# Performance work log

Hardware: AMD Instinct MI355X
Metric: run time of the kernel (lower is better)

The kernel has to match this reference:

```python
import jax, jax.numpy as jnp
import numpy as np

B, IN, OUT = 65536, 1024, 1024
NB, D, H, L = 16, 32, 64, 4      # n_bundles, bundle_dim, norm_mlp hidden, n_latent_layers
TOT = NB * D                      # total latent dim = 512 (also encoder/decoder hidden)


def setup_inputs() -> dict:
    key = jax.random.key(0)
    ks = jax.random.split(key, 20)
    rn = lambda k, shape, s=0.02: (jax.random.normal(k, shape, dtype=jnp.float32) * s)
    return {
        "x": jax.random.normal(ks[0], (B, IN), dtype=jnp.float32),
        # encoder: Linear(IN,TOT), Linear(TOT,TOT), Linear(TOT,TOT)
        "enc_w1": rn(ks[1], (TOT, IN)), "enc_b1": jnp.zeros((TOT,), jnp.float32),
        "enc_w2": rn(ks[2], (TOT, TOT)), "enc_b2": jnp.zeros((TOT,), jnp.float32),
        "enc_w3": rn(ks[3], (TOT, TOT)), "enc_b3": jnp.zeros((TOT,), jnp.float32),
        # per-latent-layer norm_mlp: Linear(NB,H)+b, Linear(H,H)+b, Linear(H,NB) no bias
        "mlp1_w": rn(ks[4], (L, H, NB)), "mlp1_b": jnp.zeros((L, H), jnp.float32),
        "mlp2_w": rn(ks[5], (L, H, H)),  "mlp2_b": jnp.zeros((L, H), jnp.float32),
        "mlp3_w": rn(ks[6], (L, NB, H)),
        # mixing_weights[i][j] has shape (d_i, d_j); homogeneous -> [L,NB,NB,D,D], init 0.01*randn
        "mix_w": rn(ks[7], (L, NB, NB, D, D), 0.01),
        "gate_bias": jnp.zeros((L, NB), jnp.float32),
        # decoder: Linear(TOT,TOT), Linear(TOT,TOT), Linear(TOT,OUT)
        "dec_w1": rn(ks[8], (TOT, TOT)), "dec_b1": jnp.zeros((TOT,), jnp.float32),
        "dec_w2": rn(ks[9], (TOT, TOT)), "dec_b2": jnp.zeros((TOT,), jnp.float32),
        "dec_w3": rn(ks[10], (OUT, TOT)), "dec_b3": jnp.zeros((OUT,), jnp.float32),
    }


def _gelu(v):
    return jax.nn.gelu(v, approximate=False)  # torch nn.GELU default (erf)


def _soft_equivariant(z, m1w, m1b, m2w, m2b, m3w, mw, gb):
    # z: [B, TOT] -> bundles [B, NB, D] (homogeneous dims, contiguous split == reshape)
    zb = z.reshape(z.shape[0], NB, D)
    norms = jnp.linalg.norm(zb, axis=-1) + 1e-8          # [B, NB]
    h = _gelu(norms @ m1w.T + m1b)                        # [B, H]
    h = _gelu(h @ m2w.T + m2b)                            # [B, H]
    scales = jax.nn.softplus(h @ m3w.T)                   # [B, NB]
    equi = zb * scales[:, :, None]                        # [B, NB, D]
    # mixed_i = sum_j F.linear(bundles[j], W[i][j]) = bundles[j] @ W[i][j].T
    mixed = jnp.einsum('bjd,ijed->bie', zb, mw)           # [B, NB, D]
    gates = jax.nn.sigmoid(gb)                            # [NB]
    combined = equi + gates[None, :, None] * mixed        # [B, NB, D]
    return z + combined.reshape(z.shape[0], TOT)          # residual


def reference(x, enc_w1, enc_b1, enc_w2, enc_b2, enc_w3, enc_b3,
              mlp1_w, mlp1_b, mlp2_w, mlp2_b, mlp3_w, mix_w, gate_bias,
              dec_w1, dec_b1, dec_w2, dec_b2, dec_w3, dec_b3):
    # encoder
    z = _gelu(x @ enc_w1.T + enc_b1)
    z = _gelu(z @ enc_w2.T + enc_b2)
    z = z @ enc_w3.T + enc_b3
    # latent dynamics: L SoftEquivariantLayers (fixed small loop over layers)
    for l in range(L):
        z = _soft_equivariant(z, mlp1_w[l], mlp1_b[l], mlp2_w[l], mlp2_b[l],
                              mlp3_w[l], mix_w[l], gate_bias[l])
    # decoder
    y = _gelu(z @ dec_w1.T + dec_b1)
    y = _gelu(y @ dec_w2.T + dec_b2)
    return y @ dec_w3.T + dec_b3
```

## Files before the change

kernel.cpp:

```cpp
#include <hip/hip_runtime.h>
#include <hip/hip_bf16.h>

typedef float f32x4 __attribute__((ext_vector_type(4)));
typedef __bf16 bf16x8 __attribute__((ext_vector_type(8)));
typedef unsigned short u16x8 __attribute__((ext_vector_type(8)));
typedef unsigned short u16;

__device__ __forceinline__ u16 f2bf(float f) {
  __bf16 h = (__bf16)f;
  return __builtin_bit_cast(u16, h);
}
__device__ __forceinline__ float bf2f(u16 s) {
  return __uint_as_float(((unsigned int)s) << 16);
}
__device__ __forceinline__ float gelu_f(float x) {
  return 0.5f * x * (1.0f + erff(x * 0.70710678118654752f));
}
__device__ __forceinline__ void gload_lds16(const void* g, void* l) {
  __builtin_amdgcn_global_load_lds((const __attribute__((address_space(1))) void*)g,
                                   (__attribute__((address_space(3))) void*)l, 16, 0, 0);
}
#define MFMA(a, b, c) __builtin_amdgcn_mfma_f32_16x16x32_bf16((a), (b), (c), 0, 0, 0)
#define BARRIER_PINNED() do { \
    __builtin_amdgcn_s_barrier(); \
    asm volatile("" ::: "memory"); \
    __builtin_amdgcn_sched_barrier(0); \
  } while (0)

__global__ void cvt_all(const float* __restrict__ e1, const float* __restrict__ e2,
                        const float* __restrict__ e3, const float* __restrict__ d1,
                        const float* __restrict__ d2, const float* __restrict__ d3,
                        const float* __restrict__ mx, u16* __restrict__ dst)
{
  int i = blockIdx.x * blockDim.x + threadIdx.x;
  int stride = gridDim.x * blockDim.x;
  for (; i < 3145728; i += stride) {
    float v;
    if (i < 524288)        v = e1[i];
    else if (i < 786432)   v = e2[i - 524288];
    else if (i < 1048576)  v = e3[i - 786432];
    else if (i < 1310720)  v = d1[i - 1048576];
    else if (i < 1572864)  v = d2[i - 1310720];
    else if (i < 2097152)  v = d3[i - 1572864];
    else {
      int j = i - 2097152;
      int l = j >> 18, rem = j & 262143;
      int o = rem >> 9, k = rem & 511;
      int bi = o >> 5, e = o & 31, jj = k >> 5, dd = k & 31;
      v = mx[(((l * 16 + bi) * 16 + jj) * 32 + e) * 32 + dd];
    }
    dst[i] = f2bf(v);
  }
}

__global__ void cvt_x(const float* __restrict__ s, u16* __restrict__ d) {
  int i = blockIdx.x * blockDim.x + threadIdx.x;
  int stride = gridDim.x * blockDim.x;
  for (; i < 8388608; i += stride) {
    float4 v0 = *(const float4*)(s + (size_t)i * 8);
    float4 v1 = *(const float4*)(s + (size_t)i * 8 + 4);
    u16x8 u;
    u[0] = f2bf(v0.x); u[1] = f2bf(v0.y); u[2] = f2bf(v0.z); u[3] = f2bf(v0.w);
    u[4] = f2bf(v1.x); u[5] = f2bf(v1.y); u[6] = f2bf(v1.z); u[7] = f2bf(v1.w);
    *(u16x8*)(d + (size_t)i * 8) = u;
  }
}

template<int EPI>
__global__ __launch_bounds__(512, 2)
void gemm_big(const u16* __restrict__ A, const u16* __restrict__ Bw,
              const float* __restrict__ bias, void* __restrict__ Cp,
              const u16* __restrict__ zOld, const float* __restrict__ scales,
              const float* __restrict__ gateBias, int M, int N, int K)
{
  extern __shared__ char smem[];
  const int tid = threadIdx.x;
  const int lane = tid & 63;
  const int wid = tid >> 6;

  const int nx = N >> 7;
  const int ny = M >> 8;
  const int d = blockIdx.x;
  const int xcd = d & 7;
  const int seq = d >> 3;
  const int by = xcd * (ny >> 3) + seq / nx;
  const int bx = seq - (seq / nx) * nx;
  const int m0 = by << 8;
  const int n0 = bx << 7;

  const int wr = wid >> 2;
  const int wc = wid & 3;
  const int r16 = lane & 15;
  const int kg = (lane >> 4) << 3;
  const int sw = (r16 & 7) << 4;

  const u16* pA[4];
  const u16* pB[2];
  #pragma unroll
  for (int it = 0; it < 4; ++it) {
    int c = ((it * 8 + wid) << 6) + lane;
    int row = c >> 3;
    int cb = (c & 7) << 4;
    pA[it] = A + (size_t)(m0 + row) * K + ((cb ^ ((row & 7) << 4)) >> 1);
  }
  #pragma unroll
  for (int it = 0; it < 2; ++it) {
    int c = ((it * 8 + wid) << 6) + lane;
    int row = c >> 3;
    int cb = (c & 7) << 4;
    pB[it] = Bw + (size_t)(n0 + row) * K + ((cb ^ ((row & 7) << 4)) >> 1);
  }

  auto stage = [&](int kt, int b) {
    char* dstA = smem + b * 49152;
    char* dstB = dstA + 32768;
    const int ko = kt << 6;
    #pragma unroll
    for (int it = 0; it < 4; ++it)
      gload_lds16(pA[it] + ko, dstA + ((it * 8 + wid) << 10));
    #pragma unroll
    for (int it = 0; it < 2; ++it)
      gload_lds16(pB[it] + ko, dstB + ((it * 8 + wid) << 10));
  };

  const int NT = K >> 6;
  f32x4 acc[8][2] = {};

  stage(0, 0);
  stage(1, 1);

  int cb = 0, ib = 2;
  for (int kt = 0; kt < NT; ++kt) {
    if (kt + 1 < NT) { asm volatile("s_waitcnt vmcnt(6)" ::: "memory"); }
    else             { asm volatile("s_waitcnt vmcnt(0)" ::: "memory"); }
    BARRIER_PINNED();

    if (kt + 2 < NT) {
      stage(kt + 2, ib);
      ib = (ib == 2) ? 0 : ib + 1;
    }

    const char* Ac = smem + cb * 49152;
    const char* Bc = Ac + 32768;
    #pragma unroll
    for (int kk = 0; kk < 64; kk += 32) {
      const int kb = ((kk + kg) << 1) ^ sw;
      bf16x8 bv0 = *(const bf16x8*)(Bc + ((wc * 32 + r16) << 7) + kb);
      bf16x8 bv1 = *(const bf16x8*)(Bc + ((wc * 32 + 16 + r16) << 7) + kb);
      #pragma unroll
      for (int mh = 0; mh < 2; ++mh) {
        bf16x8 av[4];
        #pragma unroll
        for (int m = 0; m < 4; ++m)
          av[m] = *(const bf16x8*)(Ac + ((wr * 128 + mh * 64 + m * 16 + r16) << 7) + kb);
        __builtin_amdgcn_s_setprio(1);
        #pragma unroll
        for (int m = 0; m < 4; ++m) {
          acc[mh * 4 + m][0] = MFMA(av[m], bv0, acc[mh * 4 + m][0]);
          acc[mh * 4 + m][1] = MFMA(av[m], bv1, acc[mh * 4 + m][1]);
        }
        __builtin_amdgcn_s_setprio(0);
      }
    }
    cb = (cb == 2) ? 0 : cb + 1;
  }

  const int colBase = n0 + wc * 32 + r16;
  const int rowBase = m0 + wr * 128 + ((lane >> 4) << 2);
  #pragma unroll
  for (int n = 0; n < 2; ++n) {
    const int col = colBase + n * 16;
    float bv_ = 0.f, gate = 0.f;
    if constexpr (EPI == 0 || EPI == 1 || EPI == 3) bv_ = bias[col];
    if constexpr (EPI == 2) gate = 1.f / (1.f + expf(-gateBias[col >> 5]));
    #pragma unroll
    for (int m = 0; m < 8; ++m) {
      #pragma unroll
      for (int r = 0; r < 4; ++r) {
        const int row = rowBase + m * 16 + r;
        float v = acc[m][n][r];
        if constexpr (EPI == 0) {
          ((u16*)Cp)[(size_t)row * N + col] = f2bf(gelu_f(v + bv_));
        } else if constexpr (EPI == 1) {
          ((u16*)Cp)[(size_t)row * N + col] = f2bf(v + bv_);
        } else if constexpr (EPI == 2) {
          float sc = scales[(size_t)row * 16 + (col >> 5)];
          float zo = bf2f(zOld[(size_t)row * 512 + col]);
          ((u16*)Cp)[(size_t)row * N + col] = f2bf(zo * (1.f + sc) + gate * v);
        } else {
          ((float*)Cp)[(size_t)row * N + col] = v + bv_;
        }
      }
    }
  }
}

__global__ __launch_bounds__(256, 2)
void norm_mlp2(const u16* __restrict__ z,
               const float* __restrict__ w1, const float* __restrict__ b1,
               const float* __restrict__ w2, const float* __restrict__ b2,
               const float* __restrict__ w3, float* __restrict__ scales)
{
  __shared__ float nrm[256][17];
  const int tid = threadIdx.x;
  const size_t base = (size_t)blockIdx.x << 8;

  #pragma unroll
  for (int p = 0; p < 16; ++p) {
    const int C = (p << 8) + tid;
    const int r = C >> 4, b = C & 15;
    const u16* zp = z + ((base + r) << 9) + (b << 5);
    float ss = 0.f;
    #pragma unroll
    for (int q = 0; q < 4; ++q) {
      u16x8 v = *(const u16x8*)(zp + q * 8);
      #pragma unroll
      for (int j = 0; j < 8; ++j) { float f = bf2f(v[j]); ss += f * f; }
    }
    nrm[r][b] = sqrtf(ss) + 1e-8f;
  }
  __syncthreads();

  float nr[16];
  #pragma unroll
  for (int i = 0; i < 16; ++i) nr[i] = nrm[tid][i];

  float h2[64];
  #pragma unroll
  for (int j = 0; j < 64; ++j) h2[j] = b2[j];

  for (int kt = 0; kt < 4; ++kt) {
    float h1t[16];
    #pragma unroll
    for (int k16 = 0; k16 < 16; ++k16) {
      const int k = (kt << 4) + k16;
      float t = b1[k];
      #pragma unroll
      for (int i = 0; i < 16; ++i) t += nr[i] * w1[k * 16 + i];
      h1t[k16] = gelu_f(t);
    }
    const float* w2t = w2 + (kt << 4);
    #pragma unroll
    for (int j = 0; j < 64; ++j) {
      float s = 0.f;
      #pragma unroll
      for (int k16 = 0; k16 < 16; ++k16) s += h1t[k16] * w2t[j * 64 + k16];
      h2[j] += s;
    }
  }
  #pragma unroll
  for (int j = 0; j < 64; ++j) h2[j] = gelu_f(h2[j]);

  float* srow = scales + ((base + tid) << 4);
  #pragma unroll
  for (int b = 0; b < 16; ++b) {
    float s = 0.f;
    #pragma unroll
    for (int k = 0; k < 64; ++k) s += h2[k] * w3[b * 64 + k];
    s = (s > 20.f) ? s : log1pf(expf(s));
    srow[b] = s;
  }
}

#define BIG_SMEM 147456

extern "C" void kernel_launch(void* const* d_in, const int* in_sizes, int n_in,
                              void* d_out, int out_size, void* d_ws, size_t ws_size,
                              hipStream_t stream)
{
  (void)in_sizes; (void)n_in; (void)out_size; (void)ws_size;
  const float* x      = (const float*)d_in[0];
  const float* enc_w1 = (const float*)d_in[1];
  const float* enc_b1 = (const float*)d_in[2];
  const float* enc_w2 = (const float*)d_in[3];
  const float* enc_b2 = (const float*)d_in[4];
  const float* enc_w3 = (const float*)d_in[5];
  const float* enc_b3 = (const float*)d_in[6];
  const float* mlp1_w = (const float*)d_in[7];
  const float* mlp1_b = (const float*)d_in[8];
  const float* mlp2_w = (const float*)d_in[9];
  const float* mlp2_b = (const float*)d_in[10];
  const float* mlp3_w = (const float*)d_in[11];
  const float* mix_w  = (const float*)d_in[12];
  const float* gate_b = (const float*)d_in[13];
  const float* dec_w1 = (const float*)d_in[14];
  const float* dec_b1 = (const float*)d_in[15];
  const float* dec_w2 = (const float*)d_in[16];
  const float* dec_b2 = (const float*)d_in[17];
  const float* dec_w3 = (const float*)d_in[18];
  const float* dec_b3 = (const float*)d_in[19];

  char* ws = (char*)d_ws;
  const int M = 65536;

  u16*   xb     = (u16*)ws;
  u16*   zA     = (u16*)(ws + 134217728ULL);
  u16*   zB     = (u16*)ws;
  float* scales = (float*)(ws + 201326592ULL);
  u16*   wBase  = (u16*)(ws + 205520896ULL);
  u16* wE1 = wBase;
  u16* wE2 = wE1 + 524288;
  u16* wE3 = wE2 + 262144;
  u16* wD1 = wE3 + 262144;
  u16* wD2 = wD1 + 262144;
  u16* wD3 = wD2 + 262144;
  u16* wMix = wD3 + 524288;

  hipError_t e;
  e = hipFuncSetAttribute(reinterpret_cast<const void*>(&gemm_big<0>),
                          hipFuncAttributeMaxDynamicSharedMemorySize, BIG_SMEM);
  e = hipFuncSetAttribute(reinterpret_cast<const void*>(&gemm_big<1>),
                          hipFuncAttributeMaxDynamicSharedMemorySize, BIG_SMEM);
  e = hipFuncSetAttribute(reinterpret_cast<const void*>(&gemm_big<2>),
                          hipFuncAttributeMaxDynamicSharedMemorySize, BIG_SMEM);
  e = hipFuncSetAttribute(reinterpret_cast<const void*>(&gemm_big<3>),
                          hipFuncAttributeMaxDynamicSharedMemorySize, BIG_SMEM);
  (void)e;

  cvt_all<<<512, 256, 0, stream>>>(enc_w1, enc_w2, enc_w3, dec_w1, dec_w2, dec_w3,
                                   mix_w, wBase);

  dim3 blk(512);
  const int g512  = 256 * 4;
  const int g1024 = 256 * 8;

  cvt_x<<<2048, 256, 0, stream>>>(x, xb);
  gemm_big<0><<<g512, blk, BIG_SMEM, stream>>>(xb, wE1, enc_b1, zA, nullptr, nullptr, nullptr, M, 512, 1024);
  gemm_big<0><<<g512, blk, BIG_SMEM, stream>>>(zA, wE2, enc_b2, zB, nullptr, nullptr, nullptr, M, 512, 512);
  gemm_big<1><<<g512, blk, BIG_SMEM, stream>>>(zB, wE3, enc_b3, zA, nullptr, nullptr, nullptr, M, 512, 512);

  u16* cur = zA;
  u16* nxt = zB;
  for (int l = 0; l < 4; ++l) {
    norm_mlp2<<<256, dim3(256), 0, stream>>>(cur, mlp1_w + l * 1024, mlp1_b + l * 64,
                                             mlp2_w + l * 4096, mlp2_b + l * 64,
                                             mlp3_w + l * 1024, scales);
    gemm_big<2><<<g512, blk, BIG_SMEM, stream>>>(cur, wMix + (size_t)l * 262144, nullptr, nxt,
                                                 cur, scales, gate_b + l * 16, M, 512, 512);
    u16* t = cur; cur = nxt; nxt = t;
  }

  gemm_big<0><<<g512, blk, BIG_SMEM, stream>>>(cur, wD1, dec_b1, nxt, nullptr, nullptr, nullptr, M, 512, 512);
  { u16* t = cur; cur = nxt; nxt = t; }
  gemm_big<0><<<g512, blk, BIG_SMEM, stream>>>(cur, wD2, dec_b2, nxt, nullptr, nullptr, nullptr, M, 512, 512);
  { u16* t = cur; cur = nxt; nxt = t; }
  gemm_big<3><<<g1024, blk, BIG_SMEM, stream>>>(cur, wD3, dec_b3, d_out, nullptr, nullptr, nullptr, M, 1024, 512);
}
```

Baseline: 1.199 ms.

## Widen GEMM tiles to 256x256 with double buffering and one block per CU

Switches the GEMM from 256x128 tiles with a three-stage LDS pipeline to 256x256 tiles with two-stage double buffering. Each wave now computes a 128x64 output slab with 32 accumulators, which raises MFMA work per LDS load and halves how often the A matrix is re-read from global memory. The cost is one block per CU (launch bounds 512,1), twice the accumulator registers, a full vmcnt(0) wait on every k-step, and fewer blocks in flight, so load latency may be less well hidden.

```diff
diff --git a/kernel.cpp b/kernel.cpp
--- a/kernel.cpp
+++ b/kernel.cpp
@@ -67,18 +67,18 @@
 }
 
 template<int EPI>
-__global__ __launch_bounds__(512, 2)
-void gemm_big(const u16* __restrict__ A, const u16* __restrict__ Bw,
-              const float* __restrict__ bias, void* __restrict__ Cp,
-              const u16* __restrict__ zOld, const float* __restrict__ scales,
-              const float* __restrict__ gateBias, int M, int N, int K)
+__global__ __launch_bounds__(512, 1)
+void gemm_huge(const u16* __restrict__ A, const u16* __restrict__ Bw,
+               const float* __restrict__ bias, void* __restrict__ Cp,
+               const u16* __restrict__ zOld, const float* __restrict__ scales,
+               const float* __restrict__ gateBias, int M, int N, int K)
 {
   extern __shared__ char smem[];
   const int tid = threadIdx.x;
   const int lane = tid & 63;
   const int wid = tid >> 6;
 
-  const int nx = N >> 7;
+  const int nx = N >> 8;
   const int ny = M >> 8;
   const int d = blockIdx.x;
   const int xcd = d & 7;
@@ -86,7 +86,7 @@
   const int by = xcd * (ny >> 3) + seq / nx;
   const int bx = seq - (seq / nx) * nx;
   const int m0 = by << 8;
-  const int n0 = bx << 7;
+  const int n0 = bx << 8;
 
   const int wr = wid >> 2;
   const int wc = wid & 3;
@@ -95,58 +95,49 @@
   const int sw = (r16 & 7) << 4;
 
   const u16* pA[4];
-  const u16* pB[2];
+  const u16* pB[4];
   #pragma unroll
   for (int it = 0; it < 4; ++it) {
     int c = ((it * 8 + wid) << 6) + lane;
     int row = c >> 3;
     int cb = (c & 7) << 4;
     pA[it] = A + (size_t)(m0 + row) * K + ((cb ^ ((row & 7) << 4)) >> 1);
-  }
-  #pragma unroll
-  for (int it = 0; it < 2; ++it) {
-    int c = ((it * 8 + wid) << 6) + lane;
-    int row = c >> 3;
-    int cb = (c & 7) << 4;
     pB[it] = Bw + (size_t)(n0 + row) * K + ((cb ^ ((row & 7) << 4)) >> 1);
   }
 
   auto stage = [&](int kt, int b) {
-    char* dstA = smem + b * 49152;
+    char* dstA = smem + (b << 16);
     char* dstB = dstA + 32768;
     const int ko = kt << 6;
     #pragma unroll
     for (int it = 0; it < 4; ++it)
       gload_lds16(pA[it] + ko, dstA + ((it * 8 + wid) << 10));
     #pragma unroll
-    for (int it = 0; it < 2; ++it)
+    for (int it = 0; it < 4; ++it)
       gload_lds16(pB[it] + ko, dstB + ((it * 8 + wid) << 10));
   };
 
   const int NT = K >> 6;
-  f32x4 acc[8][2] = {};
+  f32x4 acc[8][4] = {};
 
   stage(0, 0);
-  stage(1, 1);
-
-  int cb = 0, ib = 2;
+
   for (int kt = 0; kt < NT; ++kt) {
-    if (kt + 1 < NT) { asm volatile("s_waitcnt vmcnt(6)" ::: "memory"); }
-    else             { asm volatile("s_waitcnt vmcnt(0)" ::: "memory"); }
+    const int cur = kt & 1;
+    asm volatile("s_waitcnt vmcnt(0)" ::: "memory");
     BARRIER_PINNED();
 
-    if (kt + 2 < NT) {
-      stage(kt + 2, ib);
-      ib = (ib == 2) ? 0 : ib + 1;
-    }
-
-    const char* Ac = smem + cb * 49152;
+    if (kt + 1 < NT) stage(kt + 1, cur ^ 1);
+
+    const char* Ac = smem + (cur << 16);
     const char* Bc = Ac + 32768;
     #pragma unroll
     for (int kk = 0; kk < 64; kk += 32) {
       const int kb = ((kk + kg) << 1) ^ sw;
-      bf16x8 bv0 = *(const bf16x8*)(Bc + ((wc * 32 + r16) << 7) + kb);
-      bf16x8 bv1 = *(const bf16x8*)(Bc + ((wc * 32 + 16 + r16) << 7) + kb);
+      bf16x8 bv[4];
+      #pragma unroll
+      for (int n = 0; n < 4; ++n)
+        bv[n] = *(const bf16x8*)(Bc + ((wc * 64 + n * 16 + r16) << 7) + kb);
       #pragma unroll
       for (int mh = 0; mh < 2; ++mh) {
         bf16x8 av[4];
@@ -155,20 +146,19 @@
           av[m] = *(const bf16x8*)(Ac + ((wr * 128 + mh * 64 + m * 16 + r16) << 7) + kb);
         __builtin_amdgcn_s_setprio(1);
         #pragma unroll
-        for (int m = 0; m < 4; ++m) {
-          acc[mh * 4 + m][0] = MFMA(av[m], bv0, acc[mh * 4 + m][0]);
-          acc[mh * 4 + m][1] = MFMA(av[m], bv1, acc[mh * 4 + m][1]);
-        }
+        for (int m = 0; m < 4; ++m)
+          #pragma unroll
+          for (int n = 0; n < 4; ++n)
+            acc[mh * 4 + m][n] = MFMA(av[m], bv[n], acc[mh * 4 + m][n]);
         __builtin_amdgcn_s_setprio(0);
       }
     }
-    cb = (cb == 2) ? 0 : cb + 1;
-  }
-
-  const int colBase = n0 + wc * 32 + r16;
+  }
+
+  const int colBase = n0 + wc * 64 + r16;
   const int rowBase = m0 + wr * 128 + ((lane >> 4) << 2);
   #pragma unroll
-  for (int n = 0; n < 2; ++n) {
+  for (int n = 0; n < 4; ++n) {
     const int col = colBase + n * 16;
     float bv_ = 0.f, gate = 0.f;
     if constexpr (EPI == 0 || EPI == 1 || EPI == 3) bv_ = bias[col];
@@ -262,7 +252,7 @@
   }
 }
 
-#define BIG_SMEM 147456
+#define HUGE_SMEM 131072
 
 extern "C" void kernel_launch(void* const* d_in, const int* in_sizes, int n_in,
                               void* d_out, int out_size, void* d_ws, size_t ws_size,
@@ -307,27 +297,27 @@
   u16* wMix = wD3 + 524288;
 
   hipError_t e;
-  e = hipFuncSetAttribute(reinterpret_cast<const void*>(&gemm_big<0>),
-                          hipFuncAttributeMaxDynamicSharedMemorySize, BIG_SMEM);
-  e = hipFuncSetAttribute(reinterpret_cast<const void*>(&gemm_big<1>),
-                          hipFuncAttributeMaxDynamicSharedMemorySize, BIG_SMEM);
-  e = hipFuncSetAttribute(reinterpret_cast<const void*>(&gemm_big<2>),
-                          hipFuncAttributeMaxDynamicSharedMemorySize, BIG_SMEM);
-  e = hipFuncSetAttribute(reinterpret_cast<const void*>(&gemm_big<3>),
-                          hipFuncAttributeMaxDynamicSharedMemorySize, BIG_SMEM);
+  e = hipFuncSetAttribute(reinterpret_cast<const void*>(&gemm_huge<0>),
+                          hipFuncAttributeMaxDynamicSharedMemorySize, HUGE_SMEM);
+  e = hipFuncSetAttribute(reinterpret_cast<const void*>(&gemm_huge<1>),
+                          hipFuncAttributeMaxDynamicSharedMemorySize, HUGE_SMEM);
+  e = hipFuncSetAttribute(reinterpret_cast<const void*>(&gemm_huge<2>),
+                          hipFuncAttributeMaxDynamicSharedMemorySize, HUGE_SMEM);
+  e = hipFuncSetAttribute(reinterpret_cast<const void*>(&gemm_huge<3>),
+                          hipFuncAttributeMaxDynamicSharedMemorySize, HUGE_SMEM);
   (void)e;
 
   cvt_all<<<512, 256, 0, stream>>>(enc_w1, enc_w2, enc_w3, dec_w1, dec_w2, dec_w3,
                                    mix_w, wBase);
 
   dim3 blk(512);
-  const int g512  = 256 * 4;
-  const int g1024 = 256 * 8;
+  const int g512  = 256 * 2;
+  const int g1024 = 256 * 4;
 
   cvt_x<<<2048, 256, 0, stream>>>(x, xb);
-  gemm_big<0><<<g512, blk, BIG_SMEM, stream>>>(xb, wE1, enc_b1, zA, nullptr, nullptr, nullptr, M, 512, 1024);
-  gemm_big<0><<<g512, blk, BIG_SMEM, stream>>>(zA, wE2, enc_b2, zB, nullptr, nullptr, nullptr, M, 512, 512);
-  gemm_big<1><<<g512, blk, BIG_SMEM, stream>>>(zB, wE3, enc_b3, zA, nullptr, nullptr, nullptr, M, 512, 512);
+  gemm_huge<0><<<g512, blk, HUGE_SMEM, stream>>>(xb, wE1, enc_b1, zA, nullptr, nullptr, nullptr, M, 512, 1024);
+  gemm_huge<0><<<g512, blk, HUGE_SMEM, stream>>>(zA, wE2, enc_b2, zB, nullptr, nullptr, nullptr, M, 512, 512);
+  gemm_huge<1><<<g512, blk, HUGE_SMEM, stream>>>(zB, wE3, enc_b3, zA, nullptr, nullptr, nullptr, M, 512, 512);
 
   u16* cur = zA;
   u16* nxt = zB;
@@ -335,14 +325,14 @@
     norm_mlp2<<<256, dim3(256), 0, stream>>>(cur, mlp1_w + l * 1024, mlp1_b + l * 64,
                                              mlp2_w + l * 4096, mlp2_b + l * 64,
                                              mlp3_w + l * 1024, scales);
-    gemm_big<2><<<g512, blk, BIG_SMEM, stream>>>(cur, wMix + (size_t)l * 262144, nullptr, nxt,
-                                                 cur, scales, gate_b + l * 16, M, 512, 512);
+    gemm_huge<2><<<g512, blk, HUGE_SMEM, stream>>>(cur, wMix + (size_t)l * 262144, nullptr, nxt,
+                                                   cur, scales, gate_b + l * 16, M, 512, 512);
     u16* t = cur; cur = nxt; nxt = t;
   }
 
-  gemm_big<0><<<g512, blk, BIG_SMEM, stream>>>(cur, wD1, dec_b1, nxt, nullptr, nullptr, nullptr, M, 512, 512);
+  gemm_huge<0><<<g512, blk, HUGE_SMEM, stream>>>(cur, wD1, dec_b1, nxt, nullptr, nullptr, nullptr, M, 512, 512);
   { u16* t = cur; cur = nxt; nxt = t; }
-  gemm_big<0><<<g512, blk, BIG_SMEM, stream>>>(cur, wD2, dec_b2, nxt, nullptr, nullptr, nullptr, M, 512, 512);
+  gemm_huge<0><<<g512, blk, HUGE_SMEM, stream>>>(cur, wD2, dec_b2, nxt, nullptr, nullptr, nullptr, M, 512, 512);
   { u16* t = cur; cur = nxt; nxt = t; }
-  gemm_big<3><<<g1024, blk, BIG_SMEM, stream>>>(cur, wD3, dec_b3, d_out, nullptr, nullptr, nullptr, M, 1024, 512);
-}
+  gemm_huge<3><<<g1024, blk, HUGE_SMEM, stream>>>(cur, wD3, dec_b3, d_out, nullptr, nullptr, nullptr, M, 1024, 512);
+}
```

Measured after the change: 1.674 ms. 39.6% more time.
